# Optimization experiments

Hardware: AMD Instinct MI355X
Metric: run time of the kernel (lower is better)

## Reference

```python
import jax, jax.numpy as jnp
import numpy as np

N = 100000
E = 800000
HID = 128
HEADS = 4
NEG_SLOPE = 0.2


def _mlp2(x, w1, b1, w2, b2):
    h = jax.nn.relu(x @ w1.T + b1)
    return jax.nn.relu(h @ w2.T + b2)


def gat_conv(h, src, dst, lin_w, att_src, att_dst, bias, heads, out_ch, concat):
    # h: [N, in] -> hl: [N, heads, out_ch]
    n = h.shape[0]
    hl = (h @ lin_w.T).reshape(n, heads, out_ch)
    a_s = jnp.sum(hl * att_src, axis=-1)  # [N, heads]
    a_d = jnp.sum(hl * att_dst, axis=-1)
    alpha = jax.nn.leaky_relu(a_s[src] + a_d[dst], NEG_SLOPE)  # [E', heads]
    amax = jax.ops.segment_max(alpha, dst, num_segments=n)
    ex = jnp.exp(alpha - amax[dst])
    denom = jax.ops.segment_sum(ex, dst, num_segments=n)
    att = ex / denom[dst]  # segment softmax over incoming edges
    msg = hl[src] * att[:, :, None]  # [E', heads, out_ch]
    out = jax.ops.segment_sum(msg, dst, num_segments=n)
    out = out.reshape(n, heads * out_ch) if concat else out.mean(axis=1)
    return out + bias


def setup_inputs() -> dict:
    key = jax.random.key(0)
    ks = iter(jax.random.split(key, 40))
    g = lambda shape: (jax.random.normal(next(ks), shape, dtype=jnp.float32) * 0.1)
    inp = {}
    inp['x'] = jax.random.normal(next(ks), (N, 2), dtype=jnp.float32)
    inp['node_types'] = jax.random.randint(next(ks), (N,), 0, 2, dtype=jnp.int32)
    inp['edge_index'] = jax.random.randint(next(ks), (2, E), 0, N, dtype=jnp.int64)
    # heterogeneous encoder
    inp['ew1'] = g((HID, 2)); inp['eb1'] = g((HID,))
    inp['ew2'] = g((HID, HID)); inp['eb2'] = g((HID,))
    inp['cw1'] = g((HID, 1)); inp['cb1'] = g((HID,))
    inp['cw2'] = g((HID, HID)); inp['cb2'] = g((HID,))
    # GAT layers 0,1: heads=4, out_ch=HID//4, concat
    C = HID // HEADS
    inp['lin0'] = g((HID, HID)); inp['as0'] = g((HEADS, C)); inp['ad0'] = g((HEADS, C)); inp['b0'] = g((HID,))
    inp['lin1'] = g((HID, HID)); inp['as1'] = g((HEADS, C)); inp['ad1'] = g((HEADS, C)); inp['b1'] = g((HID,))
    # GAT layer 2: heads=1, out_ch=HID, concat=False
    inp['lin2'] = g((HID, HID)); inp['as2'] = g((1, HID)); inp['ad2'] = g((1, HID)); inp['b2'] = g((HID,))
    # decoder
    inp['dw1'] = g((HID, HID)); inp['db1'] = g((HID,))
    inp['dw2'] = g((HID // 2, HID)); inp['db2'] = g((HID // 2,))
    inp['dw3'] = g((1, HID // 2)); inp['db3'] = g((1,))
    return inp


def reference(x, node_types, edge_index, ew1, eb1, ew2, eb2, cw1, cb1, cw2, cb2,
              lin0, as0, ad0, b0, lin1, as1, ad1, b1, lin2, as2, ad2, b2,
              dw1, db1, dw2, db2, dw3, db3):
    n = x.shape[0]
    # heterogeneous encoding (vectorized type select)
    item_h = _mlp2(x[:, :2], ew1, eb1, ew2, eb2)
    con_h = _mlp2(x[:, :1], cw1, cb1, cw2, cb2)
    item_mask = node_types == 0
    h = jnp.where(item_mask[:, None], item_h, jnp.where((node_types == 1)[:, None], con_h, 0.0))
    # add self-loops (PyG GATConv default add_self_loops=True)
    loop = jnp.arange(n, dtype=edge_index.dtype)
    src = jnp.concatenate([edge_index[0], loop])
    dst = jnp.concatenate([edge_index[1], loop])
    C = HID // HEADS
    h0 = jax.nn.relu(gat_conv(h, src, dst, lin0, as0, ad0, b0, HEADS, C, True))
    h1 = h0 + jax.nn.relu(gat_conv(h0, src, dst, lin1, as1, ad1, b1, HEADS, C, True))
    h2 = h1 + jax.nn.relu(gat_conv(h1, src, dst, lin2, as2, ad2, b2, 1, HID, False))
    # decoder on all nodes; zero out non-item nodes (dropout is eval/no-op)
    d = jax.nn.relu(h2 @ dw1.T + db1)
    d = jax.nn.relu(d @ dw2.T + db2)
    probs = jax.nn.sigmoid(d @ dw3.T + db3).squeeze(-1)
    return probs * item_mask.astype(probs.dtype)
```

## Files before the change

### kernel.cpp

```cpp
#include <hip/hip_runtime.h>
#include <math.h>

#define HIDDEN 128
#define NEG_SLOPE 0.2f

typedef unsigned short u16;
typedef __attribute__((ext_vector_type(8))) short bf16x8;
typedef __attribute__((ext_vector_type(4))) float f32x4;

__device__ __forceinline__ u16 f2bf(float f) {
    unsigned u = __float_as_uint(f);
    unsigned r = (u + 0x7FFFu + ((u >> 16) & 1u)) >> 16;
    return (u16)r;
}
__device__ __forceinline__ float bf2f(u16 u) {
    return __uint_as_float((unsigned)u << 16);
}
__device__ __forceinline__ unsigned pack2(float a, float b) {
    return (unsigned)f2bf(a) | ((unsigned)f2bf(b) << 16);
}
__device__ __forceinline__ float lo16f(unsigned v) { return bf2f((u16)v); }
__device__ __forceinline__ float hi16f(unsigned v) { return bf2f((u16)(v >> 16)); }

struct WPtrs { const float* p[7]; };
__global__ void convw_zero_kernel(WPtrs wp, unsigned* __restrict__ wb, int totalPairs,
                                  int* __restrict__ cnt, int N) {
    int i = blockIdx.x * blockDim.x + threadIdx.x;
    if (i < N) cnt[i] = 0;
    if (i < totalPairs) {
        int e = i * 2;
        int seg, off;
        if (e < 98304) { seg = e >> 14; off = e & 16383; }
        else           { seg = 6;       off = e - 98304; }
        const float* s = wp.p[seg];
        wb[i] = pack2(s[off], s[off + 1]);
    }
}

__global__ __launch_bounds__(256) void encoder_kernel(
        const float* __restrict__ x, const int* __restrict__ types,
        const float* __restrict__ ew1, const float* __restrict__ eb1,
        const float* __restrict__ cw1, const float* __restrict__ cb1,
        const u16* __restrict__ wb_ew2, const u16* __restrict__ wb_cw2,
        const float* __restrict__ eb2, const float* __restrict__ cb2,
        u16* __restrict__ out, int N) {
    __shared__ u16 Ws[128 * 136];
    __shared__ float xsh[128];
    __shared__ float w1sh[640];
    const int tid = threadIdx.x;
    const int n0 = blockIdx.x * 64;

    if (tid < 128) {
        int n = n0 + (tid >> 1);
        xsh[tid] = (n < N) ? x[2 * n + (tid & 1)] : 0.f;
    }
    if (tid < 256) w1sh[tid] = ew1[tid];
    if (tid < 128) { w1sh[256 + tid] = eb1[tid]; w1sh[384 + tid] = cw1[tid];
                     w1sh[512 + tid] = cb1[tid]; }
#pragma unroll
    for (int r = 0; r < 8; r++) {
        int j = r * 256 + tid;
        int row = j >> 4, c8 = (j & 15) << 3;
        *(uint4*)&Ws[row * 136 + c8] = *(const uint4*)&wb_ew2[(size_t)row * 128 + c8];
    }
    __syncthreads();

    const int w = tid >> 6, lane = tid & 63;
    const int qd = lane >> 4, lr = lane & 15;
    const int row = w * 16 + lr;
    const float x0 = xsh[2 * row], x1 = xsh[2 * row + 1];

    f32x4 acc_i[8], acc_c[8];
#pragma unroll
    for (int j = 0; j < 8; j++) acc_i[j] = (f32x4){0.f, 0.f, 0.f, 0.f};

#pragma unroll
    for (int k = 0; k < 4; k++) {
        bf16x8 a;
#pragma unroll
        for (int j = 0; j < 8; j++) {
            int t = k * 32 + qd * 8 + j;
            float v = fmaxf(w1sh[2 * t] * x0 + w1sh[2 * t + 1] * x1 + w1sh[256 + t], 0.f);
            a[j] = (short)f2bf(v);
        }
#pragma unroll
        for (int j = 0; j < 8; j++) {
            bf16x8 b = *(const bf16x8*)&Ws[(j * 16 + lr) * 136 + k * 32 + qd * 8];
            acc_i[j] = __builtin_amdgcn_mfma_f32_16x16x32_bf16(a, b, acc_i[j], 0, 0, 0);
        }
    }
    __syncthreads();

#pragma unroll
    for (int r = 0; r < 8; r++) {
        int j = r * 256 + tid;
        int rw = j >> 4, c8 = (j & 15) << 3;
        *(uint4*)&Ws[rw * 136 + c8] = *(const uint4*)&wb_cw2[(size_t)rw * 128 + c8];
    }
    __syncthreads();

#pragma unroll
    for (int j = 0; j < 8; j++) acc_c[j] = (f32x4){0.f, 0.f, 0.f, 0.f};
#pragma unroll
    for (int k = 0; k < 4; k++) {
        bf16x8 a;
#pragma unroll
        for (int j = 0; j < 8; j++) {
            int t = k * 32 + qd * 8 + j;
            float v = fmaxf(w1sh[384 + t] * x0 + w1sh[512 + t], 0.f);
            a[j] = (short)f2bf(v);
        }
#pragma unroll
        for (int j = 0; j < 8; j++) {
            bf16x8 b = *(const bf16x8*)&Ws[(j * 16 + lr) * 136 + k * 32 + qd * 8];
            acc_c[j] = __builtin_amdgcn_mfma_f32_16x16x32_bf16(a, b, acc_c[j], 0, 0, 0);
        }
    }

#pragma unroll
    for (int r = 0; r < 4; r++) {
        int orow = n0 + w * 16 + qd * 4 + r;
        if (orow >= N) continue;
        int ty = types[orow];
#pragma unroll
        for (int j = 0; j < 8; j++) {
            int col = j * 16 + lr;
            float v;
            if (ty == 0)      v = fmaxf(acc_i[j][r] + eb2[col], 0.f);
            else if (ty == 1) v = fmaxf(acc_c[j][r] + cb2[col], 0.f);
            else              v = 0.f;
            out[(size_t)orow * HIDDEN + col] = f2bf(v);
        }
    }
}

template <int OUT, int DH>
__global__ __launch_bounds__(256) void gemm_mfma_kernel(
        const u16* __restrict__ X, const u16* __restrict__ Wb,
        const float* __restrict__ bias, const int* __restrict__ types,
        u16* __restrict__ out, float* __restrict__ a_s, float* __restrict__ a_d,
        const float* __restrict__ att_s, const float* __restrict__ att_d,
        const float* __restrict__ dw3, const float* __restrict__ db3,
        float* __restrict__ fout, int N, int mode) {
    constexpr int NT = OUT / 16;
    __shared__ u16 Xs[64 * 136];
    __shared__ u16 Ws[OUT * 136];
    const int tid = threadIdx.x;
    const int n0 = blockIdx.x * 64;

#pragma unroll
    for (int r = 0; r < 4; r++) {
        int j = r * 256 + tid;
        int row = j >> 4, c8 = (j & 15) << 3;
        int n = n0 + row;
        uint4 v = make_uint4(0u, 0u, 0u, 0u);
        if (n < N) v = *(const uint4*)&X[(size_t)n * 128 + c8];
        *(uint4*)&Xs[row * 136 + c8] = v;
    }
#pragma unroll
    for (int r = 0; r < NT; r++) {
        int j = r * 256 + tid;
        int row = j >> 4, c8 = (j & 15) << 3;
        *(uint4*)&Ws[row * 136 + c8] = *(const uint4*)&Wb[(size_t)row * 128 + c8];
    }
    __syncthreads();

    const int w = tid >> 6, lane = tid & 63;
    const int qd = lane >> 4, lr = lane & 15;

    f32x4 acc[NT];
#pragma unroll
    for (int j = 0; j < NT; j++) acc[j] = (f32x4){0.f, 0.f, 0.f, 0.f};

#pragma unroll
    for (int k = 0; k < 4; k++) {
        bf16x8 a = *(const bf16x8*)&Xs[(w * 16 + lr) * 136 + k * 32 + qd * 8];
#pragma unroll
        for (int j = 0; j < NT; j++) {
            bf16x8 b = *(const bf16x8*)&Ws[(j * 16 + lr) * 136 + k * 32 + qd * 8];
            acc[j] = __builtin_amdgcn_mfma_f32_16x16x32_bf16(a, b, acc[j], 0, 0, 0);
        }
    }

    if (mode == 3) {
        float pr[4] = {0.f, 0.f, 0.f, 0.f};
#pragma unroll
        for (int j = 0; j < NT; j++) {
            int col = j * 16 + lr;
            float b = bias[col], wv = dw3[col];
#pragma unroll
            for (int r = 0; r < 4; r++) pr[r] += fmaxf(acc[j][r] + b, 0.f) * wv;
        }
#pragma unroll
        for (int m = 1; m < 16; m <<= 1)
#pragma unroll
            for (int r = 0; r < 4; r++) pr[r] += __shfl_xor(pr[r], m, 64);
        if (lr == 0) {
            float b3 = db3[0];
#pragma unroll
            for (int r = 0; r < 4; r++) {
                int row = n0 + w * 16 + qd * 4 + r;
                if (row < N) {
                    float prob = 1.f / (1.f + expf(-(pr[r] + b3)));
                    fout[row] = (types[row] == 0) ? prob : 0.f;
                }
            }
        }
        return;
    }

    if (DH > 0) {
        constexpr int NH = (DH == 4) ? 4 : 1;
        float sp[NH][4], dp[NH][4];
#pragma unroll
        for (int h = 0; h < NH; h++)
#pragma unroll
            for (int r = 0; r < 4; r++) { sp[h][r] = 0.f; dp[h][r] = 0.f; }
#pragma unroll
        for (int j = 0; j < NT; j++) {
            int col = j * 16 + lr;
            float as_ = att_s[col], ad_ = att_d[col];
            int h = (DH == 4) ? (j >> 1) : 0;
#pragma unroll
            for (int r = 0; r < 4; r++) {
                sp[h][r] += acc[j][r] * as_;
                dp[h][r] += acc[j][r] * ad_;
            }
        }
#pragma unroll
        for (int m = 1; m < 16; m <<= 1)
#pragma unroll
            for (int h = 0; h < NH; h++)
#pragma unroll
                for (int r = 0; r < 4; r++) {
                    sp[h][r] += __shfl_xor(sp[h][r], m, 64);
                    dp[h][r] += __shfl_xor(dp[h][r], m, 64);
                }
        if (lr == 0) {
#pragma unroll
            for (int r = 0; r < 4; r++) {
                int row = n0 + w * 16 + qd * 4 + r;
                if (row < N) {
#pragma unroll
                    for (int h = 0; h < NH; h++) {
                        a_s[row * DH + h] = sp[h][r];
                        a_d[row * DH + h] = dp[h][r];
                    }
                }
            }
        }
    }

#pragma unroll
    for (int r = 0; r < 4; r++) {
        int row = n0 + w * 16 + qd * 4 + r;
        if (row >= N) continue;
#pragma unroll
        for (int j = 0; j < NT; j++) {
            int col = j * 16 + lr;
            float v = acc[j][r];
            if (mode >= 1) v = fmaxf(v + bias[col], 0.f);
            out[(size_t)row * OUT + col] = f2bf(v);
        }
    }
}

__global__ void hist_kernel(const int* __restrict__ ei, int E, int E2,
                            int* __restrict__ cnt, int* __restrict__ pos) {
    int e = blockIdx.x * blockDim.x + threadIdx.x;
    if (e >= E2) return;
    int d = (e < E) ? ei[E + e] : e - E;
    pos[e] = atomicAdd(&cnt[d], 1);
}

__global__ void scan1_kernel(const int* __restrict__ cnt, int* __restrict__ rs,
                             int* __restrict__ bsum, int N) {
    __shared__ int s[256];
    int i = blockIdx.x * 256 + threadIdx.x;
    int v = (i < N) ? cnt[i] : 0;
    s[threadIdx.x] = v;
    __syncthreads();
    for (int off = 1; off < 256; off <<= 1) {
        int t = (threadIdx.x >= off) ? s[threadIdx.x - off] : 0;
        __syncthreads();
        s[threadIdx.x] += t;
        __syncthreads();
    }
    if (i < N) rs[i] = s[threadIdx.x];
    if (threadIdx.x == 255) bsum[blockIdx.x] = s[255];
}

__global__ void scan23_kernel(int* __restrict__ rs, const int* __restrict__ cnt,
                              const int* __restrict__ bsum, int N) {
    __shared__ int sdata[256];
    int b = blockIdx.x;
    int partial = 0;
    for (int i = threadIdx.x; i < b; i += 256) partial += bsum[i];
    sdata[threadIdx.x] = partial;
    __syncthreads();
    for (int off = 128; off; off >>= 1) {
        if (threadIdx.x < off) sdata[threadIdx.x] += sdata[threadIdx.x + off];
        __syncthreads();
    }
    int pre = sdata[0];
    int i = b * 256 + threadIdx.x;
    if (i < N) rs[i] = rs[i] - cnt[i] + pre;
}

__global__ void scatter_kernel(const int* __restrict__ ei, int E, int E2,
                               const int* __restrict__ rs, const int* __restrict__ pos,
                               int* __restrict__ srclist) {
    int e = blockIdx.x * blockDim.x + threadIdx.x;
    if (e >= E2) return;
    int s, d;
    if (e < E) { s = ei[e]; d = ei[E + e]; }
    else       { s = d = e - E; }
    srclist[rs[d] + pos[e]] = s;
}

template <int H>
__global__ void att_kernel(const int* __restrict__ rs, const int* __restrict__ cnt,
                           const int* __restrict__ srclist,
                           const float* __restrict__ a_s, const float* __restrict__ a_d,
                           float* __restrict__ ex, float* __restrict__ dinv, int N) {
    int i = blockIdx.x * blockDim.x + threadIdx.x;
    if (i >= N * H) return;
    int n = (H == 1) ? i : (i >> 2);
    int h = (H == 1) ? 0 : (i & 3);
    int beg = rs[n], deg = cnt[n];
    float ad = a_d[i];
    float l = 0.f;
    for (int k = 0; k < deg; k++) {
        float al = a_s[srclist[beg + k] * H + h] + ad;
        al = (al > 0.f) ? al : NEG_SLOPE * al;
        float p = expf(fminf(al, 80.f));
        ex[(beg + k) * H + h] = p;
        l += p;
    }
    dinv[i] = 1.f / l;
}

template <int H>
__global__ __launch_bounds__(256) void gat_agg_kernel(
        const int* __restrict__ rs, const int* __restrict__ cnt,
        const int* __restrict__ srclist, const u16* __restrict__ hl,
        const float* __restrict__ ex, const float* __restrict__ dinv,
        const float* __restrict__ bias, const u16* __restrict__ res,
        u16* __restrict__ out, int N) {
    int n = blockIdx.x * 4 + (threadIdx.x >> 6);
    int l = threadIdx.x & 63;
    if (n >= N) return;
    const int g = l >> 4;
    const int c = l & 15;
    const int head = (H == 1) ? 0 : (c >> 2);
    const int beg = rs[n];
    const int deg = cnt[n];
    float acc0[8], acc1[8], acc2[8];
#pragma unroll
    for (int j = 0; j < 8; j++) { acc0[j] = 0.f; acc1[j] = 0.f; acc2[j] = 0.f; }

    for (int k = 0; k < deg; k += 12) {
        int i0 = k + g, i1 = k + 4 + g, i2 = k + 8 + g;
        int e0 = beg + min(i0, deg - 1);
        int e1 = beg + min(i1, deg - 1);
        int e2 = beg + min(i2, deg - 1);
        int s0 = srclist[e0], s1 = srclist[e1], s2 = srclist[e2];
        float p0 = ex[e0 * H + head];
        float p1 = ex[e1 * H + head];
        float p2 = ex[e2 * H + head];
        if (i0 >= deg) p0 = 0.f;
        if (i1 >= deg) p1 = 0.f;
        if (i2 >= deg) p2 = 0.f;
        uint4 v0 = *(const uint4*)&hl[(size_t)s0 * 128 + 8 * c];
        uint4 v1 = *(const uint4*)&hl[(size_t)s1 * 128 + 8 * c];
        uint4 v2 = *(const uint4*)&hl[(size_t)s2 * 128 + 8 * c];
        acc0[0] += p0 * lo16f(v0.x); acc0[1] += p0 * hi16f(v0.x);
        acc0[2] += p0 * lo16f(v0.y); acc0[3] += p0 * hi16f(v0.y);
        acc0[4] += p0 * lo16f(v0.z); acc0[5] += p0 * hi16f(v0.z);
        acc0[6] += p0 * lo16f(v0.w); acc0[7] += p0 * hi16f(v0.w);
        acc1[0] += p1 * lo16f(v1.x); acc1[1] += p1 * hi16f(v1.x);
        acc1[2] += p1 * lo16f(v1.y); acc1[3] += p1 * hi16f(v1.y);
        acc1[4] += p1 * lo16f(v1.z); acc1[5] += p1 * hi16f(v1.z);
        acc1[6] += p1 * lo16f(v1.w); acc1[7] += p1 * hi16f(v1.w);
        acc2[0] += p2 * lo16f(v2.x); acc2[1] += p2 * hi16f(v2.x);
        acc2[2] += p2 * lo16f(v2.y); acc2[3] += p2 * hi16f(v2.y);
        acc2[4] += p2 * lo16f(v2.z); acc2[5] += p2 * hi16f(v2.z);
        acc2[6] += p2 * lo16f(v2.w); acc2[7] += p2 * hi16f(v2.w);
    }
#pragma unroll
    for (int j = 0; j < 8; j++) {
        float a = acc0[j] + acc1[j] + acc2[j];
        a += __shfl_xor(a, 16, 64);
        a += __shfl_xor(a, 32, 64);
        acc0[j] = a;
    }
    if (g == 0) {
        float di = dinv[n * H + head];
        float4 b0 = *(const float4*)&bias[8 * c];
        float4 b1 = *(const float4*)&bias[8 * c + 4];
        float o[8];
        o[0] = fmaxf(acc0[0] * di + b0.x, 0.f);
        o[1] = fmaxf(acc0[1] * di + b0.y, 0.f);
        o[2] = fmaxf(acc0[2] * di + b0.z, 0.f);
        o[3] = fmaxf(acc0[3] * di + b0.w, 0.f);
        o[4] = fmaxf(acc0[4] * di + b1.x, 0.f);
        o[5] = fmaxf(acc0[5] * di + b1.y, 0.f);
        o[6] = fmaxf(acc0[6] * di + b1.z, 0.f);
        o[7] = fmaxf(acc0[7] * di + b1.w, 0.f);
        if (res) {
            uint4 rv = *(const uint4*)&res[(size_t)n * 128 + 8 * c];
            o[0] += lo16f(rv.x); o[1] += hi16f(rv.x);
            o[2] += lo16f(rv.y); o[3] += hi16f(rv.y);
            o[4] += lo16f(rv.z); o[5] += hi16f(rv.z);
            o[6] += lo16f(rv.w); o[7] += hi16f(rv.w);
        }
        uint4 ov = make_uint4(pack2(o[0], o[1]), pack2(o[2], o[3]),
                              pack2(o[4], o[5]), pack2(o[6], o[7]));
        *(uint4*)&out[(size_t)n * 128 + 8 * c] = ov;
    }
}

template <int H>
static void gat_layer(const u16* X, const u16* lin, const float* as_, const float* ad_,
                      const float* bias, const u16* res, u16* hl, u16* outb,
                      float* a_s, float* a_d, float* ex, float* dinv,
                      const int* rs, const int* cnt, const int* srclist,
                      int N, hipStream_t stream) {
    int gx = (N + 63) / 64;
    gemm_mfma_kernel<128, H><<<gx, 256, 0, stream>>>(
        X, lin, nullptr, nullptr, hl, a_s, a_d, as_, ad_, nullptr, nullptr, nullptr, N, 0);
    att_kernel<H><<<(N * H + 255) / 256, 256, 0, stream>>>(rs, cnt, srclist, a_s, a_d,
                                                           ex, dinv, N);
    gat_agg_kernel<H><<<(N + 3) / 4, 256, 0, stream>>>(rs, cnt, srclist, hl, ex, dinv,
                                                       bias, res, outb, N);
}

extern "C" void kernel_launch(void* const* d_in, const int* in_sizes, int n_in,
                              void* d_out, int out_size, void* d_ws, size_t ws_size,
                              hipStream_t stream) {
    const float* x     = (const float*)d_in[0];
    const int*   types = (const int*)d_in[1];
    const int*   ei    = (const int*)d_in[2];
    const float* ew1 = (const float*)d_in[3];
    const float* eb1 = (const float*)d_in[4];
    const float* ew2 = (const float*)d_in[5];
    const float* eb2 = (const float*)d_in[6];
    const float* cw1 = (const float*)d_in[7];
    const float* cb1 = (const float*)d_in[8];
    const float* cw2 = (const float*)d_in[9];
    const float* cb2 = (const float*)d_in[10];
    const float* lin0 = (const float*)d_in[11];
    const float* as0  = (const float*)d_in[12];
    const float* ad0  = (const float*)d_in[13];
    const float* b0   = (const float*)d_in[14];
    const float* lin1 = (const float*)d_in[15];
    const float* as1  = (const float*)d_in[16];
    const float* ad1  = (const float*)d_in[17];
    const float* b1   = (const float*)d_in[18];
    const float* lin2 = (const float*)d_in[19];
    const float* as2  = (const float*)d_in[20];
    const float* ad2  = (const float*)d_in[21];
    const float* b2   = (const float*)d_in[22];
    const float* dw1 = (const float*)d_in[23];
    const float* db1 = (const float*)d_in[24];
    const float* dw2 = (const float*)d_in[25];
    const float* db2 = (const float*)d_in[26];
    const float* dw3 = (const float*)d_in[27];
    const float* db3 = (const float*)d_in[28];

    int N  = in_sizes[1];
    int E  = in_sizes[2] / 2;
    int E2 = E + N;

    size_t NF = (size_t)N * HIDDEN;
    u16* bufA = (u16*)d_ws;
    u16* bufB = bufA + NF;
    u16* bufC = bufB + NF;
    float* fbase = (float*)(bufC + NF);
    float* a_s  = fbase;
    float* a_d  = a_s + (size_t)N * 4;
    float* dinv = a_d + (size_t)N * 4;
    float* ex   = dinv + (size_t)N * 4;
    int* rs      = (int*)(ex + (size_t)E2 * 4);
    int* cnt     = rs + N;
    int* pos     = cnt + N;
    int* bsum    = pos + E2;
    int* srclist = bsum + 1024;
    u16* wb      = (u16*)(srclist + E2);
    u16* wb_ew2  = wb;
    u16* wb_cw2  = wb + 16384;
    u16* wb_lin0 = wb + 32768;
    u16* wb_lin1 = wb + 49152;
    u16* wb_lin2 = wb + 65536;
    u16* wb_dw1  = wb + 81920;
    u16* wb_dw2  = wb + 98304;

    int nb = (N + 255) / 256;

    WPtrs wp;
    wp.p[0] = ew2; wp.p[1] = cw2; wp.p[2] = lin0; wp.p[3] = lin1;
    wp.p[4] = lin2; wp.p[5] = dw1; wp.p[6] = dw2;
    int cz = max(N, 53248);
    convw_zero_kernel<<<(cz + 255) / 256, 256, 0, stream>>>(wp, (unsigned*)wb, 53248,
                                                            cnt, N);

    hist_kernel<<<(E2 + 255) / 256, 256, 0, stream>>>(ei, E, E2, cnt, pos);
    scan1_kernel<<<nb, 256, 0, stream>>>(cnt, rs, bsum, N);
    scan23_kernel<<<nb, 256, 0, stream>>>(rs, cnt, bsum, N);
    scatter_kernel<<<(E2 + 255) / 256, 256, 0, stream>>>(ei, E, E2, rs, pos, srclist);

    int gx = (N + 63) / 64;

    encoder_kernel<<<gx, 256, 0, stream>>>(x, types, ew1, eb1, cw1, cb1,
                                           wb_ew2, wb_cw2, eb2, cb2, bufA, N);

    gat_layer<4>(bufA, wb_lin0, as0, ad0, b0, nullptr, bufB, bufA,
                 a_s, a_d, ex, dinv, rs, cnt, srclist, N, stream);
    gat_layer<4>(bufA, wb_lin1, as1, ad1, b1, bufA, bufB, bufC,
                 a_s, a_d, ex, dinv, rs, cnt, srclist, N, stream);
    gat_layer<1>(bufC, wb_lin2, as2, ad2, b2, bufC, bufB, bufA,
                 a_s, a_d, ex, dinv, rs, cnt, srclist, N, stream);

    gemm_mfma_kernel<128, 0><<<gx, 256, 0, stream>>>(
        bufA, wb_dw1, db1, nullptr, bufC, nullptr, nullptr, nullptr, nullptr,
        nullptr, nullptr, nullptr, N, 1);
    gemm_mfma_kernel<64, 0><<<gx, 256, 0, stream>>>(
        bufC, wb_dw2, db2, types, nullptr, nullptr, nullptr, nullptr, nullptr,
        dw3, db3, (float*)d_out, N, 3);
}
```

Measured before the change: 510.0 us.

## Fuse attention softmax computation into GAT aggregation kernel

Removes the separate attention kernel that computed per-edge exp weights and per-node inverse denominators. The aggregation kernel now gathers a_s per source, applies leaky-relu and fast exp inline, and accumulates the denominator alongside the weighted features, reducing it with shuffles. This drops one launch per layer and the write and read of the per-edge ex buffer. In exchange each edge recomputes exp in 16 lanes per wavefront group, and the kernel uses the faster, less precise __expf.

```diff
diff --git a/kernel.cpp b/kernel.cpp
--- a/kernel.cpp
+++ b/kernel.cpp
@@ -319,32 +319,10 @@
 }
 
 template <int H>
-__global__ void att_kernel(const int* __restrict__ rs, const int* __restrict__ cnt,
-                           const int* __restrict__ srclist,
-                           const float* __restrict__ a_s, const float* __restrict__ a_d,
-                           float* __restrict__ ex, float* __restrict__ dinv, int N) {
-    int i = blockIdx.x * blockDim.x + threadIdx.x;
-    if (i >= N * H) return;
-    int n = (H == 1) ? i : (i >> 2);
-    int h = (H == 1) ? 0 : (i & 3);
-    int beg = rs[n], deg = cnt[n];
-    float ad = a_d[i];
-    float l = 0.f;
-    for (int k = 0; k < deg; k++) {
-        float al = a_s[srclist[beg + k] * H + h] + ad;
-        al = (al > 0.f) ? al : NEG_SLOPE * al;
-        float p = expf(fminf(al, 80.f));
-        ex[(beg + k) * H + h] = p;
-        l += p;
-    }
-    dinv[i] = 1.f / l;
-}
-
-template <int H>
 __global__ __launch_bounds__(256) void gat_agg_kernel(
         const int* __restrict__ rs, const int* __restrict__ cnt,
         const int* __restrict__ srclist, const u16* __restrict__ hl,
-        const float* __restrict__ ex, const float* __restrict__ dinv,
+        const float* __restrict__ a_s, const float* __restrict__ a_d,
         const float* __restrict__ bias, const u16* __restrict__ res,
         u16* __restrict__ out, int N) {
     int n = blockIdx.x * 4 + (threadIdx.x >> 6);
@@ -355,7 +333,9 @@
     const int head = (H == 1) ? 0 : (c >> 2);
     const int beg = rs[n];
     const int deg = cnt[n];
+    const float ad = a_d[n * H + head];
     float acc0[8], acc1[8], acc2[8];
+    float den0 = 0.f, den1 = 0.f, den2 = 0.f;
 #pragma unroll
     for (int j = 0; j < 8; j++) { acc0[j] = 0.f; acc1[j] = 0.f; acc2[j] = 0.f; }
 
@@ -365,12 +345,19 @@
         int e1 = beg + min(i1, deg - 1);
         int e2 = beg + min(i2, deg - 1);
         int s0 = srclist[e0], s1 = srclist[e1], s2 = srclist[e2];
-        float p0 = ex[e0 * H + head];
-        float p1 = ex[e1 * H + head];
-        float p2 = ex[e2 * H + head];
+        float al0 = a_s[s0 * H + head] + ad;
+        float al1 = a_s[s1 * H + head] + ad;
+        float al2 = a_s[s2 * H + head] + ad;
+        al0 = (al0 > 0.f) ? al0 : NEG_SLOPE * al0;
+        al1 = (al1 > 0.f) ? al1 : NEG_SLOPE * al1;
+        al2 = (al2 > 0.f) ? al2 : NEG_SLOPE * al2;
+        float p0 = __expf(fminf(al0, 80.f));
+        float p1 = __expf(fminf(al1, 80.f));
+        float p2 = __expf(fminf(al2, 80.f));
         if (i0 >= deg) p0 = 0.f;
         if (i1 >= deg) p1 = 0.f;
         if (i2 >= deg) p2 = 0.f;
+        den0 += p0; den1 += p1; den2 += p2;
         uint4 v0 = *(const uint4*)&hl[(size_t)s0 * 128 + 8 * c];
         uint4 v1 = *(const uint4*)&hl[(size_t)s1 * 128 + 8 * c];
         uint4 v2 = *(const uint4*)&hl[(size_t)s2 * 128 + 8 * c];
@@ -394,8 +381,11 @@
         a += __shfl_xor(a, 32, 64);
         acc0[j] = a;
     }
+    float den = den0 + den1 + den2;
+    den += __shfl_xor(den, 16, 64);
+    den += __shfl_xor(den, 32, 64);
     if (g == 0) {
-        float di = dinv[n * H + head];
+        float di = 1.f / den;
         float4 b0 = *(const float4*)&bias[8 * c];
         float4 b1 = *(const float4*)&bias[8 * c + 4];
         float o[8];
@@ -423,15 +413,13 @@
 template <int H>
 static void gat_layer(const u16* X, const u16* lin, const float* as_, const float* ad_,
                       const float* bias, const u16* res, u16* hl, u16* outb,
-                      float* a_s, float* a_d, float* ex, float* dinv,
+                      float* a_s, float* a_d,
                       const int* rs, const int* cnt, const int* srclist,
                       int N, hipStream_t stream) {
     int gx = (N + 63) / 64;
     gemm_mfma_kernel<128, H><<<gx, 256, 0, stream>>>(
         X, lin, nullptr, nullptr, hl, a_s, a_d, as_, ad_, nullptr, nullptr, nullptr, N, 0);
-    att_kernel<H><<<(N * H + 255) / 256, 256, 0, stream>>>(rs, cnt, srclist, a_s, a_d,
-                                                           ex, dinv, N);
-    gat_agg_kernel<H><<<(N + 3) / 4, 256, 0, stream>>>(rs, cnt, srclist, hl, ex, dinv,
+    gat_agg_kernel<H><<<(N + 3) / 4, 256, 0, stream>>>(rs, cnt, srclist, hl, a_s, a_d,
                                                        bias, res, outb, N);
 }
 
@@ -479,9 +467,7 @@
     float* fbase = (float*)(bufC + NF);
     float* a_s  = fbase;
     float* a_d  = a_s + (size_t)N * 4;
-    float* dinv = a_d + (size_t)N * 4;
-    float* ex   = dinv + (size_t)N * 4;
-    int* rs      = (int*)(ex + (size_t)E2 * 4);
+    int* rs      = (int*)(a_d + (size_t)N * 4);
     int* cnt     = rs + N;
     int* pos     = cnt + N;
     int* bsum    = pos + E2;
@@ -515,11 +501,11 @@
                                            wb_ew2, wb_cw2, eb2, cb2, bufA, N);
 
     gat_layer<4>(bufA, wb_lin0, as0, ad0, b0, nullptr, bufB, bufA,
-                 a_s, a_d, ex, dinv, rs, cnt, srclist, N, stream);
+                 a_s, a_d, rs, cnt, srclist, N, stream);
     gat_layer<4>(bufA, wb_lin1, as1, ad1, b1, bufA, bufB, bufC,
-                 a_s, a_d, ex, dinv, rs, cnt, srclist, N, stream);
+                 a_s, a_d, rs, cnt, srclist, N, stream);
     gat_layer<1>(bufC, wb_lin2, as2, ad2, b2, bufC, bufB, bufA,
-                 a_s, a_d, ex, dinv, rs, cnt, srclist, N, stream);
+                 a_s, a_d, rs, cnt, srclist, N, stream);
 
     gemm_mfma_kernel<128, 0><<<gx, 256, 0, stream>>>(
         bufA, wb_dw1, db1, nullptr, bufC, nullptr, nullptr, nullptr, nullptr,
```

Result: faster. 483.6 us (-5.2%).
